# Optimization experiments

Hardware: AMD Instinct MI355X
Metric: run time of the kernel (lower is better)

## Reference

```python
import jax, jax.numpy as jnp
import numpy as np


def setup_inputs() -> dict:
    key = jax.random.key(0)
    k1, k2, k3 = jax.random.split(key, 3)
    B, S, K, N = 4, 2048, 4096, 4096
    x = jax.random.normal(k1, (B, S, K), dtype=jnp.float16)
    # int8 weight codes in [-128, 127]
    w_int8 = jax.random.randint(k2, (N, K), -128, 128, dtype=jnp.int32).astype(jnp.int8)
    # per-output-row weight scale (positive, smallish like abs-max/127 of fp weights)
    weight_scale = (jax.random.uniform(k3, (N,), dtype=jnp.float32) + 0.5) * 0.01
    matmul_out_scale = jnp.full((1,), 1.0 / 1024.0, dtype=jnp.float32)
    return {"x": x, "w_int8": w_int8, "weight_scale": weight_scale,
            "matmul_out_scale": matmul_out_scale}


def reference(x, w_int8, weight_scale, matmul_out_scale):
    B, S, K = x.shape
    xf = x.astype(jnp.float32)
    # dynamic per-token symmetric int8 quantization (TOKEN_INT8_127)
    x_scales = jnp.max(jnp.abs(xf), axis=-1, keepdims=True) / 127.0  # [B,S,1] float32
    x_int8 = jnp.clip(jnp.round(xf / x_scales), -128, 127).astype(jnp.int8)
    x_scales_h = x_scales[..., 0].astype(jnp.float16)  # [B,S]
    y = jnp.einsum('mk,nk->mn', x_int8.reshape(-1, K), w_int8,
                   preferred_element_type=jnp.int32).astype(jnp.float32)
    y = y.reshape(B, S, -1)
    y = (y * matmul_out_scale[0]).astype(jnp.float16)
    # fp16 * fp32 -> fp32 (matches torch type promotion); per-row and per-token dequant
    out = y * weight_scale * x_scales_h[:, :, None]
    return out
```

## Files before the change

kernel.cpp:

```cpp
#include <hip/hip_runtime.h>
#include <hip/hip_fp16.h>
#include <stdint.h>

typedef int v4i __attribute__((ext_vector_type(4)));

#define GLOAD_LDS16(g, l) __builtin_amdgcn_global_load_lds(                  \
    (const __attribute__((address_space(1))) void*)(g),                      \
    (__attribute__((address_space(3))) void*)(l), 16, 0, 0)

#define XQ_OFF 0u
#define XS_OFF 33554432u
#define W8_OFF 33570816u

__device__ inline bool x_is_f32(const void* xin) {
  const uint32_t* xw = (const uint32_t*)xin;
  bool ok = true;
  #pragma unroll
  for (int i = 0; i < 16; ++i) ok &= ((xw[i] & 0x1FFFu) == 0u);
  return ok;
}
__device__ inline bool w_is_i32(const void* win) {
  const int* wi = (const int*)win;
  bool ok = true;
  #pragma unroll
  for (int i = 0; i < 16; ++i) ok &= (wi[i] >= -128 && wi[i] <= 127);
  return ok;
}

__global__ __launch_bounds__(256) void repack_w(
    const void* __restrict__ win, int8_t* __restrict__ w8, int total)
{
  const bool as32 = w_is_i32(win);
  const int tid  = blockIdx.x * 256 + threadIdx.x;
  const int nthr = gridDim.x * 256;
  if (as32) {
    const int4* w4 = (const int4*)win;
    uint32_t* dst = (uint32_t*)w8;
    const int n4 = total >> 2;
    for (int i = tid; i < n4; i += nthr) {
      int4 v = w4[i];
      dst[i] = (uint32_t)(v.x & 255) | ((uint32_t)(v.y & 255) << 8) |
               ((uint32_t)(v.z & 255) << 16) | ((uint32_t)(v.w & 255) << 24);
    }
  } else {
    const uint4* src = (const uint4*)win;
    uint4* dst = (uint4*)w8;
    const int n16 = total >> 4;
    for (int i = tid; i < n16; i += nthr) dst[i] = src[i];
  }
}

__global__ __launch_bounds__(256) void quant_rows(
    const void* __restrict__ xin, int8_t* __restrict__ xq,
    __half* __restrict__ xs, int K)
{
  const bool xf32 = x_is_f32(xin);
  const int row  = blockIdx.x;
  const int tid  = threadIdx.x;
  const int lane = tid & 63;
  const int wv   = tid >> 6;
  const size_t base = (size_t)row * (size_t)K;
  __shared__ float wmax[4];

  if (xf32 && K == 4096) {
    const float4* x4 = (const float4*)((const float*)xin + base);
    float4 v[4];
    #pragma unroll
    for (int i = 0; i < 4; ++i) v[i] = x4[i * 256 + tid];
    float mx = 0.0f;
    #pragma unroll
    for (int i = 0; i < 4; ++i)
      mx = fmaxf(mx, fmaxf(fmaxf(fabsf(v[i].x), fabsf(v[i].y)),
                           fmaxf(fabsf(v[i].z), fabsf(v[i].w))));
    #pragma unroll
    for (int off = 32; off; off >>= 1) mx = fmaxf(mx, __shfl_xor(mx, off, 64));
    if (lane == 0) wmax[wv] = mx;
    __syncthreads();
    const float scale =
        fmaxf(fmaxf(wmax[0], wmax[1]), fmaxf(wmax[2], wmax[3])) / 127.0f;
    if (tid == 0) xs[row] = __float2half(scale);
    uint32_t* q = (uint32_t*)(xq + base);
    #pragma unroll
    for (int i = 0; i < 4; ++i) {
      float f[4] = {v[i].x, v[i].y, v[i].z, v[i].w};
      uint32_t p = 0;
      #pragma unroll
      for (int j = 0; j < 4; ++j) {
        float r = fminf(127.0f, fmaxf(-128.0f, rintf(f[j] / scale)));
        p |= ((uint32_t)((int)r & 255)) << (8 * j);
      }
      q[i * 256 + tid] = p;
    }
    return;
  }

  float mx = 0.0f;
  if (xf32) {
    const float* x = (const float*)xin + base;
    for (int k = tid * 4; k < K; k += 256 * 4) {
      float4 v = *(const float4*)(x + k);
      mx = fmaxf(mx, fmaxf(fmaxf(fabsf(v.x), fabsf(v.y)),
                           fmaxf(fabsf(v.z), fabsf(v.w))));
    }
  } else {
    const __half* x = (const __half*)xin + base;
    for (int k = tid * 8; k < K; k += 256 * 8) {
      uint4 u = *(const uint4*)(x + k);
      const __half* hp = (const __half*)&u;
      #pragma unroll
      for (int j = 0; j < 8; ++j) mx = fmaxf(mx, fabsf(__half2float(hp[j])));
    }
  }
  #pragma unroll
  for (int off = 32; off; off >>= 1) mx = fmaxf(mx, __shfl_xor(mx, off, 64));
  if (lane == 0) wmax[wv] = mx;
  __syncthreads();
  const float scale =
      fmaxf(fmaxf(wmax[0], wmax[1]), fmaxf(wmax[2], wmax[3])) / 127.0f;
  if (tid == 0) xs[row] = __float2half(scale);

  for (int k = tid * 8; k < K; k += 256 * 8) {
    float f[8];
    if (xf32) {
      const float* x = (const float*)xin + base;
      float4 a = *(const float4*)(x + k);
      float4 b = *(const float4*)(x + k + 4);
      f[0]=a.x; f[1]=a.y; f[2]=a.z; f[3]=a.w; f[4]=b.x; f[5]=b.y; f[6]=b.z; f[7]=b.w;
    } else {
      const __half* x = (const __half*)xin + base;
      uint4 u = *(const uint4*)(x + k);
      const __half* hp = (const __half*)&u;
      #pragma unroll
      for (int j = 0; j < 8; ++j) f[j] = __half2float(hp[j]);
    }
    uint32_t p0 = 0, p1 = 0;
    #pragma unroll
    for (int j = 0; j < 4; ++j) {
      float r = fminf(127.0f, fmaxf(-128.0f, rintf(f[j] / scale)));
      p0 |= ((uint32_t)((int)r & 255)) << (8 * j);
    }
    #pragma unroll
    for (int j = 0; j < 4; ++j) {
      float r = fminf(127.0f, fmaxf(-128.0f, rintf(f[4 + j] / scale)));
      p1 |= ((uint32_t)((int)r & 255)) << (8 * j);
    }
    uint2 st; st.x = p0; st.y = p1;
    *(uint2*)(xq + base + k) = st;
  }
}

__global__ __launch_bounds__(512, 2) void gemm_w8a8(
    const int8_t* __restrict__ xq, const int8_t* __restrict__ wq,
    const __half* __restrict__ xs, const float* __restrict__ wscale,
    const float* __restrict__ mos, float* __restrict__ out,
    int M, int N, int K)
{
  __shared__ int8_t sA[2][256 * 128];
  __shared__ int8_t sB[2][256 * 128];

  const int tid  = threadIdx.x;
  const int lane = tid & 63;
  const int w    = tid >> 6;
  const int wr   = w >> 2;
  const int wc   = w & 3;
  const int lr   = lane & 15;
  const int lk   = lane >> 4;

  int L = blockIdx.x;
  const int nwg = gridDim.x;
  if ((nwg & 7) == 0) L = (L & 7) * (nwg >> 3) + (L >> 3);
  const int ntn = N >> 8;
  const int bn = (L % ntn) << 8;
  const int bm = (L / ntn) << 8;

  v4i acc[8][4];
  #pragma unroll
  for (int i = 0; i < 8; ++i)
    #pragma unroll
    for (int j = 0; j < 4; ++j) {
      v4i z = {0, 0, 0, 0};
      acc[i][j] = z;
    }

  auto stageA = [&](int kt, int buf) {
    const int k0 = kt << 7;
    #pragma unroll
    for (int i = 0; i < 4; ++i) {
      const int li = i * 512 + tid;
      const int r  = li >> 3;
      const int p  = li & 7;
      const int sc = p ^ (r & 7);
      GLOAD_LDS16(xq + (size_t)(bm + r) * K + k0 + (sc << 4),
                  &sA[buf][(i * 512 + (w << 6)) << 4]);
    }
  };
  auto stageB = [&](int kt, int buf) {
    const int k0 = kt << 7;
    #pragma unroll
    for (int i = 0; i < 4; ++i) {
      const int li = i * 512 + tid;
      const int r  = li >> 3;
      const int p  = li & 7;
      const int sc = p ^ (r & 7);
      GLOAD_LDS16(wq + (size_t)(bn + r) * K + k0 + (sc << 4),
                  &sB[buf][(i * 512 + (w << 6)) << 4]);
    }
  };

  const int rowA0 = (wr << 7) + lr;
  const int aoff0 = rowA0 * 128 + ((lk ^ (lr & 7)) << 4);
  const int aoff1 = aoff0 ^ 64;
  const int rowB0 = (wc << 6) + lr;
  const int boff0 = rowB0 * 128 + ((lk ^ (lr & 7)) << 4);
  const int boff1 = boff0 ^ 64;

  const int nt = K >> 7;

  stageA(0, 0); stageB(0, 0);
  asm volatile("s_waitcnt vmcnt(0)" ::: "memory");
  __builtin_amdgcn_s_barrier();

  #pragma unroll 1
  for (int t = 0; t < nt; ++t) {
    const int buf = t & 1;
    const int8_t* Ab = sA[buf];
    const int8_t* Bb = sB[buf];
    const bool do_stage = (t + 1 < nt);
    v4i a00[4], a10[4], a01[4], a11[4], b0[4], b1[4];

    #pragma unroll
    for (int j = 0; j < 4; ++j) a00[j] = *(const v4i*)(Ab + aoff0 + j * 2048);
    #pragma unroll
    for (int j = 0; j < 4; ++j) b0[j]  = *(const v4i*)(Bb + boff0 + j * 2048);

    if (do_stage) stageA(t + 1, buf ^ 1);

    asm volatile("s_waitcnt lgkmcnt(0)" ::: "memory");
    __builtin_amdgcn_s_setprio(1);
    #pragma unroll
    for (int j = 0; j < 4; ++j)
      #pragma unroll
      for (int ni = 0; ni < 4; ++ni)
        acc[j][ni] = __builtin_amdgcn_mfma_i32_16x16x64_i8(
            a00[j], b0[ni], acc[j][ni], 0, 0, 0);
    __builtin_amdgcn_s_setprio(0);

    #pragma unroll
    for (int j = 0; j < 4; ++j) a10[j] = *(const v4i*)(Ab + aoff0 + 8192 + j * 2048);
    #pragma unroll
    for (int j = 0; j < 4; ++j) b1[j]  = *(const v4i*)(Bb + boff1 + j * 2048);
    #pragma unroll
    for (int j = 0; j < 4; ++j) a01[j] = *(const v4i*)(Ab + aoff1 + j * 2048);

    if (do_stage) stageB(t + 1, buf ^ 1);

    asm volatile("s_waitcnt lgkmcnt(8)" ::: "memory");
    __builtin_amdgcn_s_setprio(1);
    #pragma unroll
    for (int j = 0; j < 4; ++j)
      #pragma unroll
      for (int ni = 0; ni < 4; ++ni)
        acc[4 + j][ni] = __builtin_amdgcn_mfma_i32_16x16x64_i8(
            a10[j], b0[ni], acc[4 + j][ni], 0, 0, 0);
    __builtin_amdgcn_s_setprio(0);

    #pragma unroll
    for (int j = 0; j < 4; ++j) a11[j] = *(const v4i*)(Ab + aoff1 + 8192 + j * 2048);

    asm volatile("s_waitcnt lgkmcnt(4)" ::: "memory");
    __builtin_amdgcn_s_setprio(1);
    #pragma unroll
    for (int j = 0; j < 4; ++j)
      #pragma unroll
      for (int ni = 0; ni < 4; ++ni)
        acc[j][ni] = __builtin_amdgcn_mfma_i32_16x16x64_i8(
            a01[j], b1[ni], acc[j][ni], 0, 0, 0);
    __builtin_amdgcn_s_setprio(0);

    asm volatile("s_waitcnt lgkmcnt(0)" ::: "memory");
    __builtin_amdgcn_s_setprio(1);
    #pragma unroll
    for (int j = 0; j < 4; ++j)
      #pragma unroll
      for (int ni = 0; ni < 4; ++ni)
        acc[4 + j][ni] = __builtin_amdgcn_mfma_i32_16x16x64_i8(
            a11[j], b1[ni], acc[4 + j][ni], 0, 0, 0);
    __builtin_amdgcn_s_setprio(0);

    asm volatile("s_waitcnt vmcnt(0)" ::: "memory");
    __builtin_amdgcn_s_barrier();
  }

  const float s_out = mos[0];
  #pragma unroll
  for (int ni = 0; ni < 4; ++ni) {
    const int n_g = bn + (wc << 6) + ni * 16 + lr;
    const float wsc = wscale[n_g];
    #pragma unroll
    for (int mi = 0; mi < 8; ++mi) {
      #pragma unroll
      for (int j = 0; j < 4; ++j) {
        const int m_g = bm + (wr << 7) + mi * 16 + lk * 4 + j;
        const float y = __half2float(__float2half((float)acc[mi][ni][j] * s_out));
        out[(size_t)m_g * N + n_g] = (y * wsc) * __half2float(xs[m_g]);
      }
    }
  }
}

extern "C" void kernel_launch(void* const* d_in, const int* in_sizes, int n_in,
                              void* d_out, int out_size, void* d_ws, size_t ws_size,
                              hipStream_t stream) {
  const void*  x      = d_in[0];
  const void*  win    = d_in[1];
  const float* wscale = (const float*)d_in[2];
  const float* mos    = (const float*)d_in[3];
  float*       out    = (float*)d_out;

  const int N = in_sizes[2];
  const int K = in_sizes[1] / N;
  const int M = in_sizes[0] / K;

  int8_t* xq = (int8_t*)d_ws + XQ_OFF;
  __half* xs = (__half*)((char*)d_ws + XS_OFF);
  int8_t* w8 = (int8_t*)d_ws + W8_OFF;

  repack_w<<<2048, 256, 0, stream>>>(win, w8, N * K);
  quant_rows<<<M, 256, 0, stream>>>(x, xq, xs, K);

  gemm_w8a8<<<dim3((M >> 8) * (N >> 8)), 512, 0, stream>>>(
      xq, w8, xs, wscale, mos, out, M, N, K);
}
```

Before: 190.1 us.

## Switch GEMM to 32x32x32 int8 MFMA and merge prologue kernels

Replaces the 16x16x64 int8 MFMA tiling with 32x32x32 MFMA instructions. This roughly halves the LDS fragment reads per unit of compute and regroups the K-loop into four k-substeps with software-pipelined register double buffering. It also merges the weight repack and per-token quantization kernels into one launch, using a split block range. The trade-offs are more accumulator registers per instruction and an epilogue with a less contiguous store pattern.

New measurement: 213.7 us. +12.4%, slower.

```diff
diff --git a/kernel.cpp b/kernel.cpp
--- a/kernel.cpp
+++ b/kernel.cpp
@@ -2,7 +2,8 @@
 #include <hip/hip_fp16.h>
 #include <stdint.h>
 
-typedef int v4i __attribute__((ext_vector_type(4)));
+typedef int v4i  __attribute__((ext_vector_type(4)));
+typedef int v16i __attribute__((ext_vector_type(16)));
 
 #define GLOAD_LDS16(g, l) __builtin_amdgcn_global_load_lds(                  \
     (const __attribute__((address_space(1))) void*)(g),                      \
@@ -27,36 +28,40 @@
   return ok;
 }
 
-__global__ __launch_bounds__(256) void repack_w(
-    const void* __restrict__ win, int8_t* __restrict__ w8, int total)
+#define RW_BLOCKS 1024
+
+__global__ __launch_bounds__(256) void prologue(
+    const void* __restrict__ xin, const void* __restrict__ win,
+    int8_t* __restrict__ xq, __half* __restrict__ xs,
+    int8_t* __restrict__ w8, int K, int M, int wtotal)
 {
-  const bool as32 = w_is_i32(win);
-  const int tid  = blockIdx.x * 256 + threadIdx.x;
-  const int nthr = gridDim.x * 256;
-  if (as32) {
-    const int4* w4 = (const int4*)win;
-    uint32_t* dst = (uint32_t*)w8;
-    const int n4 = total >> 2;
-    for (int i = tid; i < n4; i += nthr) {
-      int4 v = w4[i];
-      dst[i] = (uint32_t)(v.x & 255) | ((uint32_t)(v.y & 255) << 8) |
-               ((uint32_t)(v.z & 255) << 16) | ((uint32_t)(v.w & 255) << 24);
-    }
-  } else {
-    const uint4* src = (const uint4*)win;
-    uint4* dst = (uint4*)w8;
-    const int n16 = total >> 4;
-    for (int i = tid; i < n16; i += nthr) dst[i] = src[i];
-  }
-}
-
-__global__ __launch_bounds__(256) void quant_rows(
-    const void* __restrict__ xin, int8_t* __restrict__ xq,
-    __half* __restrict__ xs, int K)
-{
+  const int tid = threadIdx.x;
+
+  if (blockIdx.x >= (unsigned)M) {
+    const bool as32 = w_is_i32(win);
+    const int bid  = blockIdx.x - M;
+    const int gtid = bid * 256 + tid;
+    const int nthr = RW_BLOCKS * 256;
+    if (as32) {
+      const int4* w4 = (const int4*)win;
+      uint32_t* dst = (uint32_t*)w8;
+      const int n4 = wtotal >> 2;
+      for (int i = gtid; i < n4; i += nthr) {
+        int4 v = w4[i];
+        dst[i] = (uint32_t)(v.x & 255) | ((uint32_t)(v.y & 255) << 8) |
+                 ((uint32_t)(v.z & 255) << 16) | ((uint32_t)(v.w & 255) << 24);
+      }
+    } else {
+      const uint4* src = (const uint4*)win;
+      uint4* dst = (uint4*)w8;
+      const int n16 = wtotal >> 4;
+      for (int i = gtid; i < n16; i += nthr) dst[i] = src[i];
+    }
+    return;
+  }
+
   const bool xf32 = x_is_f32(xin);
   const int row  = blockIdx.x;
-  const int tid  = threadIdx.x;
   const int lane = tid & 63;
   const int wv   = tid >> 6;
   const size_t base = (size_t)row * (size_t)K;
@@ -163,8 +168,8 @@
   const int w    = tid >> 6;
   const int wr   = w >> 2;
   const int wc   = w & 3;
-  const int lr   = lane & 15;
-  const int lk   = lane >> 4;
+  const int l31  = lane & 31;
+  const int hk   = lane >> 5;
 
   int L = blockIdx.x;
   const int nwg = gridDim.x;
@@ -173,14 +178,13 @@
   const int bn = (L % ntn) << 8;
   const int bm = (L / ntn) << 8;
 
-  v4i acc[8][4];
-  #pragma unroll
-  for (int i = 0; i < 8; ++i)
-    #pragma unroll
-    for (int j = 0; j < 4; ++j) {
-      v4i z = {0, 0, 0, 0};
-      acc[i][j] = z;
-    }
+  v16i acc[4][2];
+  #pragma unroll
+  for (int i = 0; i < 4; ++i)
+    #pragma unroll
+    for (int j = 0; j < 2; ++j)
+      #pragma unroll
+      for (int r = 0; r < 16; ++r) acc[i][j][r] = 0;
 
   auto stageA = [&](int kt, int buf) {
     const int k0 = kt << 7;
@@ -207,18 +211,34 @@
     }
   };
 
-  const int rowA0 = (wr << 7) + lr;
-  const int aoff0 = rowA0 * 128 + ((lk ^ (lr & 7)) << 4);
-  const int aoff1 = aoff0 ^ 64;
-  const int rowB0 = (wc << 6) + lr;
-  const int boff0 = rowB0 * 128 + ((lk ^ (lr & 7)) << 4);
-  const int boff1 = boff0 ^ 64;
+  const int rowA0 = (wr << 7) + l31;
+  const int aoffb = rowA0 * 128 + (((hk) ^ (lane & 7)) << 4);
+  const int rowB0 = (wc << 6) + l31;
+  const int boffb = rowB0 * 128 + (((hk) ^ (lane & 7)) << 4);
 
   const int nt = K >> 7;
 
   stageA(0, 0); stageB(0, 0);
   asm volatile("s_waitcnt vmcnt(0)" ::: "memory");
   __builtin_amdgcn_s_barrier();
+
+#define READ_KS(AV, BV, KS)                                                  \
+    _Pragma("unroll")                                                        \
+    for (int mt = 0; mt < 4; ++mt)                                           \
+      AV[mt] = *(const v4i*)(Ab + ((aoffb ^ ((KS) << 5)) + mt * 4096));      \
+    _Pragma("unroll")                                                        \
+    for (int nl = 0; nl < 2; ++nl)                                           \
+      BV[nl] = *(const v4i*)(Bb + ((boffb ^ ((KS) << 5)) + nl * 4096));
+
+#define MFMA_KS(AV, BV)                                                      \
+    __builtin_amdgcn_s_setprio(1);                                           \
+    _Pragma("unroll")                                                        \
+    for (int mt = 0; mt < 4; ++mt)                                           \
+      _Pragma("unroll")                                                      \
+      for (int nl = 0; nl < 2; ++nl)                                         \
+        acc[mt][nl] = __builtin_amdgcn_mfma_i32_32x32x32_i8(                 \
+            AV[mt], BV[nl], acc[mt][nl], 0, 0, 0);                           \
+    __builtin_amdgcn_s_setprio(0);
 
   #pragma unroll 1
   for (int t = 0; t < nt; ++t) {
@@ -226,82 +246,44 @@
     const int8_t* Ab = sA[buf];
     const int8_t* Bb = sB[buf];
     const bool do_stage = (t + 1 < nt);
-    v4i a00[4], a10[4], a01[4], a11[4], b0[4], b1[4];
-
-    #pragma unroll
-    for (int j = 0; j < 4; ++j) a00[j] = *(const v4i*)(Ab + aoff0 + j * 2048);
-    #pragma unroll
-    for (int j = 0; j < 4; ++j) b0[j]  = *(const v4i*)(Bb + boff0 + j * 2048);
-
+    v4i A0[4], A1[4], B0[2], B1[2];
+
+    READ_KS(A0, B0, 0)
     if (do_stage) stageA(t + 1, buf ^ 1);
+    READ_KS(A1, B1, 1)
+    asm volatile("s_waitcnt lgkmcnt(6)" ::: "memory");
+    MFMA_KS(A0, B0)
+
+    if (do_stage) stageB(t + 1, buf ^ 1);
+    READ_KS(A0, B0, 2)
+    asm volatile("s_waitcnt lgkmcnt(6)" ::: "memory");
+    MFMA_KS(A1, B1)
+
+    READ_KS(A1, B1, 3)
+    asm volatile("s_waitcnt lgkmcnt(6)" ::: "memory");
+    MFMA_KS(A0, B0)
 
     asm volatile("s_waitcnt lgkmcnt(0)" ::: "memory");
-    __builtin_amdgcn_s_setprio(1);
-    #pragma unroll
-    for (int j = 0; j < 4; ++j)
-      #pragma unroll
-      for (int ni = 0; ni < 4; ++ni)
-        acc[j][ni] = __builtin_amdgcn_mfma_i32_16x16x64_i8(
-            a00[j], b0[ni], acc[j][ni], 0, 0, 0);
-    __builtin_amdgcn_s_setprio(0);
-
-    #pragma unroll
-    for (int j = 0; j < 4; ++j) a10[j] = *(const v4i*)(Ab + aoff0 + 8192 + j * 2048);
-    #pragma unroll
-    for (int j = 0; j < 4; ++j) b1[j]  = *(const v4i*)(Bb + boff1 + j * 2048);
-    #pragma unroll
-    for (int j = 0; j < 4; ++j) a01[j] = *(const v4i*)(Ab + aoff1 + j * 2048);
-
-    if (do_stage) stageB(t + 1, buf ^ 1);
-
-    asm volatile("s_waitcnt lgkmcnt(8)" ::: "memory");
-    __builtin_amdgcn_s_setprio(1);
-    #pragma unroll
-    for (int j = 0; j < 4; ++j)
-      #pragma unroll
-      for (int ni = 0; ni < 4; ++ni)
-        acc[4 + j][ni] = __builtin_amdgcn_mfma_i32_16x16x64_i8(
-            a10[j], b0[ni], acc[4 + j][ni], 0, 0, 0);
-    __builtin_amdgcn_s_setprio(0);
-
-    #pragma unroll
-    for (int j = 0; j < 4; ++j) a11[j] = *(const v4i*)(Ab + aoff1 + 8192 + j * 2048);
-
-    asm volatile("s_waitcnt lgkmcnt(4)" ::: "memory");
-    __builtin_amdgcn_s_setprio(1);
-    #pragma unroll
-    for (int j = 0; j < 4; ++j)
-      #pragma unroll
-      for (int ni = 0; ni < 4; ++ni)
-        acc[j][ni] = __builtin_amdgcn_mfma_i32_16x16x64_i8(
-            a01[j], b1[ni], acc[j][ni], 0, 0, 0);
-    __builtin_amdgcn_s_setprio(0);
-
-    asm volatile("s_waitcnt lgkmcnt(0)" ::: "memory");
-    __builtin_amdgcn_s_setprio(1);
-    #pragma unroll
-    for (int j = 0; j < 4; ++j)
-      #pragma unroll
-      for (int ni = 0; ni < 4; ++ni)
-        acc[4 + j][ni] = __builtin_amdgcn_mfma_i32_16x16x64_i8(
-            a11[j], b1[ni], acc[4 + j][ni], 0, 0, 0);
-    __builtin_amdgcn_s_setprio(0);
+    MFMA_KS(A1, B1)
 
     asm volatile("s_waitcnt vmcnt(0)" ::: "memory");
     __builtin_amdgcn_s_barrier();
   }
 
+#undef READ_KS
+#undef MFMA_KS
+
   const float s_out = mos[0];
   #pragma unroll
-  for (int ni = 0; ni < 4; ++ni) {
-    const int n_g = bn + (wc << 6) + ni * 16 + lr;
+  for (int nl = 0; nl < 2; ++nl) {
+    const int n_g = bn + (wc << 6) + nl * 32 + l31;
     const float wsc = wscale[n_g];
     #pragma unroll
-    for (int mi = 0; mi < 8; ++mi) {
-      #pragma unroll
-      for (int j = 0; j < 4; ++j) {
-        const int m_g = bm + (wr << 7) + mi * 16 + lk * 4 + j;
-        const float y = __half2float(__float2half((float)acc[mi][ni][j] * s_out));
+    for (int mt = 0; mt < 4; ++mt) {
+      #pragma unroll
+      for (int r = 0; r < 16; ++r) {
+        const int m_g = bm + (wr << 7) + mt * 32 + (r & 3) + 8 * (r >> 2) + 4 * hk;
+        const float y = __half2float(__float2half((float)acc[mt][nl][r] * s_out));
         out[(size_t)m_g * N + n_g] = (y * wsc) * __half2float(xs[m_g]);
       }
     }
@@ -325,8 +307,7 @@
   __half* xs = (__half*)((char*)d_ws + XS_OFF);
   int8_t* w8 = (int8_t*)d_ws + W8_OFF;
 
-  repack_w<<<2048, 256, 0, stream>>>(win, w8, N * K);
-  quant_rows<<<M, 256, 0, stream>>>(x, xq, xs, K);
+  prologue<<<M + RW_BLOCKS, 256, 0, stream>>>(x, win, xq, xs, w8, K, M, N * K);
 
   gemm_w8a8<<<dim3((M >> 8) * (N >> 8)), 512, 0, stream>>>(
       xq, w8, xs, wscale, mos, out, M, N, K);
```
